# Optimization experiments

Hardware: AMD Instinct MI355X
Metric: run time of the kernel (lower is better)

Reference implementation:

```python
import jax, jax.numpy as jnp
import numpy as np

RADIUS = 0.2  # radius_cutoff
EPS_H = 1e-6
EPS_T = 1e-8
NUM_KNOTS = 16


def setup_inputs() -> dict:
    key = jax.random.key(0)
    ks = jax.random.split(key, 10)
    B, N, C = 2, 48 * 48, 16
    x = jax.random.normal(ks[0], (B, N, C), jnp.float32)
    phi_w1 = jax.random.normal(ks[1], (4, 32), jnp.float32) * 0.5
    phi_b1 = jax.random.normal(ks[2], (32,), jnp.float32) * 0.1
    phi_w2 = jax.random.normal(ks[3], (32, 1), jnp.float32) * 0.2
    phi_b2 = jax.random.normal(ks[4], (1,), jnp.float32) * 0.1
    h_w1 = jax.random.normal(ks[5], (2, 32), jnp.float32) * 0.5
    h_b1 = jax.random.normal(ks[6], (32,), jnp.float32) * 0.1
    h_w2 = jax.random.normal(ks[7], (32, 1), jnp.float32) * 0.2
    h_b2 = jax.random.normal(ks[8], (1,), jnp.float32) * 0.1
    S_m = jax.random.normal(ks[9], (NUM_KNOTS,), jnp.float32)
    return dict(x=x, phi_w1=phi_w1, phi_b1=phi_b1, phi_w2=phi_w2, phi_b2=phi_b2,
                h_w1=h_w1, h_b1=h_b1, h_w2=h_w2, h_b2=h_b2, S_m=S_m)


def _radial_spline(r, S_m):
    K = S_m.shape[0]
    knots = jnp.linspace(0.0, 1.0, K)
    r = jnp.clip(r, 0.0, 1.0)
    idx = jnp.clip(jnp.floor(r * (K - 1)).astype(jnp.int32), 0, K - 2)
    t_k = knots[idx]
    t_k1 = knots[idx + 1]
    wr = (r - t_k) / (t_k1 - t_k + EPS_T)
    return (1.0 - wr) * S_m[idx] + wr * S_m[idx + 1]


def reference(x, phi_w1, phi_b1, phi_w2, phi_b2, h_w1, h_b1, h_w2, h_b2, S_m):
    B, N, C = x.shape
    H = int(N ** 0.5)
    lin = jnp.linspace(0.0, 1.0, H)
    gx, gy = jnp.meshgrid(lin, lin, indexing='ij')
    coords = jnp.stack([gx, gy], axis=-1).reshape(N, 2)  # identical for every batch element

    # dense pairwise distances + radius mask  [N, N]
    diff = coords[:, None, :] - coords[None, :, :]
    dist = jnp.sqrt(jnp.sum(diff * diff, axis=-1))
    mask = (dist <= RADIUS).astype(x.dtype)

    # h_net: per-query bandwidth, Softplus(Linear(ReLU(Linear(coords))))  [N]
    h = jax.nn.softplus(jax.nn.relu(coords @ h_w1 + h_b1) @ h_w2 + h_b2)[:, 0]
    r_scaled = dist / (h[:, None] + EPS_H)
    psi = _radial_spline(r_scaled, S_m) * mask  # [N, N]

    # phi_net on all (x_i, y_j) coord pairs; original only fills masked entries,
    # elsewhere phi stays 0 -> dense eval then mask is the same math.  [N, N]
    xy = jnp.concatenate([jnp.broadcast_to(coords[:, None, :], (N, N, 2)),
                          jnp.broadcast_to(coords[None, :, :], (N, N, 2))], axis=-1)
    phi = (jax.nn.relu(xy @ phi_w1 + phi_b1) @ phi_w2 + phi_b2)[..., 0] * mask

    weights = phi * psi  # [N, N], same for every batch element
    norm = jnp.maximum(jnp.sum(mask, axis=-1, keepdims=True), 1.0)  # [N, 1]
    # sum_j weights[i,j] * x[b,j,c] / norm[i]  -- avoids materializing [B,N,N,C]
    out = jnp.einsum('ij,bjc->bic', weights, x) / norm[None, :, :]
    return out
```

## Files before the change

kernel.cpp:

```cpp
#include <hip/hip_runtime.h>
#include <cmath>

namespace {
constexpr int HG = 48;
constexpr int NP = HG * HG;
constexpr int CH = 16;
constexpr int WIN = 19;
constexpr int WIN2 = WIN * WIN;
constexpr float RADIUS = 0.2f;
constexpr float EPS_H = 1e-6f;
constexpr float EPS_T = 1e-8f;
constexpr int KNOTS = 16;
constexpr int PPB = 4;
constexpr int NCAND = 6;
}

__device__ __forceinline__ float lin48(int t) {
    return (t == HG - 1) ? 1.0f : (float)t * (1.0f / 47.0f);
}

__device__ __forceinline__ float softplus_f(float v) {
    return fmaxf(v, 0.0f) + log1pf(expf(-fabsf(v)));
}

__device__ __forceinline__ void wave_lds_fence() {
    __asm__ volatile("s_waitcnt lgkmcnt(0)" ::: "memory");
}

__global__ __launch_bounds__(256)
void si_blocks_kernel(const float* __restrict__ x,
                      const float* __restrict__ phi_w1,
                      const float* __restrict__ phi_b1,
                      const float* __restrict__ phi_w2,
                      const float* __restrict__ phi_b2,
                      const float* __restrict__ h_w1,
                      const float* __restrict__ h_b1,
                      const float* __restrict__ h_w2,
                      const float* __restrict__ h_b2,
                      const float* __restrict__ S_m,
                      float* __restrict__ out)
{
    const int tid  = threadIdx.x;
    const int lane = tid & 63;
    const int wv   = tid >> 6;
    const int i    = blockIdx.x * PPB + wv;
    const int ri   = i / HG;
    const int ci   = i - ri * HG;
    const float xi = lin48(ri);
    const float yi = lin48(ci);

    __shared__ float4 s_pq[PPB][32];
    __shared__ float  s_Sm[PPB][KNOTS];
    __shared__ float  s_w[PPB][WIN2];

    if (lane < 32) {
        const float pre = xi * phi_w1[lane] + yi * phi_w1[32 + lane] + phi_b1[lane];
        s_pq[wv][lane] = make_float4(pre, phi_w1[64 + lane], phi_w1[96 + lane],
                                     phi_w2[lane]);
    }
    if (lane < KNOTS) s_Sm[wv][lane] = S_m[lane];

    float hval;
    {
        const int k = lane & 31;
        float t = fmaxf(xi * h_w1[k] + yi * h_w1[32 + k] + h_b1[k], 0.0f) * h_w2[k];
        #pragma unroll
        for (int m = 1; m < 32; m <<= 1) t += __shfl_xor(t, m, 64);
        hval = softplus_f(t + h_b2[0]) + EPS_H;
    }
    const float b2    = phi_b2[0];
    const float rhinv = 1.0f / hval;

    wave_lds_fence();

    float xjv[NCAND], yjv[NCAND], pw[NCAND], accp[NCAND];
    float cnt = 0.0f;

    #pragma unroll
    for (int s = 0; s < NCAND; ++s) {
        const int t  = lane + 64 * s;
        const int tt = (t < WIN2) ? t : 0;
        const int a  = tt / WIN;
        const int bb = tt - a * WIN;
        const int rj = ri + a - 9;
        const int cj = ci + bb - 9;
        const bool valid = (t < WIN2) &&
                           ((unsigned)rj < (unsigned)HG) &&
                           ((unsigned)cj < (unsigned)HG);
        const int rjc = min(max(rj, 0), HG - 1);
        const int cjc = min(max(cj, 0), HG - 1);
        const float xx = lin48(rjc);
        const float yy = lin48(cjc);
        const float dx = xi - xx;
        const float dy = yi - yy;
        const float dist = sqrtf(dx * dx + dy * dy);
        const float m = (valid && dist <= RADIUS) ? 1.0f : 0.0f;
        cnt += m;

        float r = fminf(dist * rhinv, 1.0f);
        int idx = (int)(r * (float)(KNOTS - 1));
        idx = idx > (KNOTS - 2) ? (KNOTS - 2) : idx;
        const float tk  = (float)idx * (1.0f / (float)(KNOTS - 1));
        const float tk1 = (idx == KNOTS - 2) ? 1.0f
                        : (float)(idx + 1) * (1.0f / (float)(KNOTS - 1));
        const float wr  = (r - tk) / (tk1 - tk + EPS_T);
        const float psi = (1.0f - wr) * s_Sm[wv][idx] + wr * s_Sm[wv][idx + 1];

        pw[s]   = psi * m;
        xjv[s]  = xx;
        yjv[s]  = yy;
        accp[s] = b2;
    }

    #pragma unroll
    for (int m = 1; m < 64; m <<= 1) cnt += __shfl_xor(cnt, m, 64);
    const float rnorm = 1.0f / fmaxf(cnt, 1.0f);

    #pragma unroll
    for (int k = 0; k < 32; ++k) {
        const float4 q = s_pq[wv][k];
        #pragma unroll
        for (int s = 0; s < NCAND; ++s) {
            const float hk = fmaf(xjv[s], q.y, fmaf(yjv[s], q.z, q.x));
            accp[s] = fmaf(fmaxf(hk, 0.0f), q.w, accp[s]);
        }
    }

    #pragma unroll
    for (int s = 0; s < NCAND; ++s) {
        const int t = lane + 64 * s;
        if (t < WIN2) s_w[wv][t] = accp[s] * pw[s] * rnorm;
    }

    wave_lds_fence();

    const int rep = lane >> 3;
    const int pc  = lane & 7;
    const int b   = pc >> 2;
    const int c4  = pc & 3;
    const float* xb = x + b * NP * CH + c4 * 4;

    float4 acc = make_float4(0.0f, 0.0f, 0.0f, 0.0f);
    int t = rep, a = 0, bb = rep;
    #pragma unroll 8
    for (int n = 0; n < 46; ++n) {
        if (t < WIN2) {
            const int rj  = ri + a - 9;
            const int cj  = ci + bb - 9;
            const int rjc = min(max(rj, 0), HG - 1);
            const int cjc = min(max(cj, 0), HG - 1);
            const int j   = rjc * HG + cjc;
            const float wgt = s_w[wv][t];
            const float4 xv = *(const float4*)(xb + j * CH);
            acc.x = fmaf(wgt, xv.x, acc.x);
            acc.y = fmaf(wgt, xv.y, acc.y);
            acc.z = fmaf(wgt, xv.z, acc.z);
            acc.w = fmaf(wgt, xv.w, acc.w);
        }
        t += 8;
        bb += 8;
        const int ov = (bb >= WIN) ? 1 : 0;
        bb -= ov * WIN;
        a  += ov;
    }

    #pragma unroll
    for (int off = 8; off < 64; off <<= 1) {
        acc.x += __shfl_down(acc.x, off, 64);
        acc.y += __shfl_down(acc.y, off, 64);
        acc.z += __shfl_down(acc.z, off, 64);
        acc.w += __shfl_down(acc.w, off, 64);
    }

    if (rep == 0) {
        *(float4*)(out + (size_t)(b * NP + i) * CH + c4 * 4) = acc;
    }
}

extern "C" void kernel_launch(void* const* d_in, const int* in_sizes, int n_in,
                              void* d_out, int out_size, void* d_ws, size_t ws_size,
                              hipStream_t stream) {
    const float* x      = (const float*)d_in[0];
    const float* phi_w1 = (const float*)d_in[1];
    const float* phi_b1 = (const float*)d_in[2];
    const float* phi_w2 = (const float*)d_in[3];
    const float* phi_b2 = (const float*)d_in[4];
    const float* h_w1   = (const float*)d_in[5];
    const float* h_b1   = (const float*)d_in[6];
    const float* h_w2   = (const float*)d_in[7];
    const float* h_b2   = (const float*)d_in[8];
    const float* S_m    = (const float*)d_in[9];
    float* out          = (float*)d_out;

    si_blocks_kernel<<<dim3(NP / PPB), dim3(256), 0, stream>>>(
        x, phi_w1, phi_b1, phi_w2, phi_b2,
        h_w1, h_b1, h_w2, h_b2, S_m, out);
}
```

Before: 88.78 us.

## Use one 256-thread block per query point instead of one wave per point

Each block now handles a single query point, and its four waves share the 361-entry window. Weight computation is split across 256 threads (2 candidates each instead of 6), the neighbour count uses ballot/popcount, and the gather loop is split across waves with a cross-wave LDS reduction and a final normalise. The aim is to shorten the per-point critical path and launch 4x more blocks for parallelism. In exchange it adds block-wide barriers and recomputes the h_net and shared setup four times as often.

```diff
diff --git a/kernel.cpp b/kernel.cpp
--- a/kernel.cpp
+++ b/kernel.cpp
@@ -11,8 +11,6 @@
 constexpr float EPS_H = 1e-6f;
 constexpr float EPS_T = 1e-8f;
 constexpr int KNOTS = 16;
-constexpr int PPB = 4;
-constexpr int NCAND = 6;
 }
 
 __device__ __forceinline__ float lin48(int t) {
@@ -21,10 +19,6 @@
 
 __device__ __forceinline__ float softplus_f(float v) {
     return fmaxf(v, 0.0f) + log1pf(expf(-fabsf(v)));
-}
-
-__device__ __forceinline__ void wave_lds_fence() {
-    __asm__ volatile("s_waitcnt lgkmcnt(0)" ::: "memory");
 }
 
 __global__ __launch_bounds__(256)
@@ -43,22 +37,24 @@
     const int tid  = threadIdx.x;
     const int lane = tid & 63;
     const int wv   = tid >> 6;
-    const int i    = blockIdx.x * PPB + wv;
+    const int i    = blockIdx.x;
     const int ri   = i / HG;
     const int ci   = i - ri * HG;
     const float xi = lin48(ri);
     const float yi = lin48(ci);
 
-    __shared__ float4 s_pq[PPB][32];
-    __shared__ float  s_Sm[PPB][KNOTS];
-    __shared__ float  s_w[PPB][WIN2];
+    __shared__ float4 s_pq[32];
+    __shared__ float  s_Sm[KNOTS];
+    __shared__ float  s_w[WIN2];
+    __shared__ float4 s_part[4][8];
+    __shared__ float  s_cnt[4];
 
-    if (lane < 32) {
-        const float pre = xi * phi_w1[lane] + yi * phi_w1[32 + lane] + phi_b1[lane];
-        s_pq[wv][lane] = make_float4(pre, phi_w1[64 + lane], phi_w1[96 + lane],
-                                     phi_w2[lane]);
+    if (tid < 32) {
+        const float pre = xi * phi_w1[tid] + yi * phi_w1[32 + tid] + phi_b1[tid];
+        s_pq[tid] = make_float4(pre, phi_w1[64 + tid], phi_w1[96 + tid], phi_w2[tid]);
+    } else if (tid < 32 + KNOTS) {
+        s_Sm[tid - 32] = S_m[tid - 32];
     }
-    if (lane < KNOTS) s_Sm[wv][lane] = S_m[lane];
 
     float hval;
     {
@@ -68,25 +64,23 @@
         for (int m = 1; m < 32; m <<= 1) t += __shfl_xor(t, m, 64);
         hval = softplus_f(t + h_b2[0]) + EPS_H;
     }
+    const float rhinv = 1.0f / hval;
     const float b2    = phi_b2[0];
-    const float rhinv = 1.0f / hval;
 
-    wave_lds_fence();
+    __syncthreads();
 
-    float xjv[NCAND], yjv[NCAND], pw[NCAND], accp[NCAND];
     float cnt = 0.0f;
-
     #pragma unroll
-    for (int s = 0; s < NCAND; ++s) {
-        const int t  = lane + 64 * s;
-        const int tt = (t < WIN2) ? t : 0;
+    for (int s = 0; s < 2; ++s) {
+        const int t  = tid + 256 * s;
+        const bool in = (t < WIN2);
+        const int tt = in ? t : 0;
         const int a  = tt / WIN;
         const int bb = tt - a * WIN;
         const int rj = ri + a - 9;
         const int cj = ci + bb - 9;
-        const bool valid = (t < WIN2) &&
-                           ((unsigned)rj < (unsigned)HG) &&
-                           ((unsigned)cj < (unsigned)HG);
+        const bool valid = in && ((unsigned)rj < (unsigned)HG) &&
+                                 ((unsigned)cj < (unsigned)HG);
         const int rjc = min(max(rj, 0), HG - 1);
         const int cjc = min(max(cj, 0), HG - 1);
         const float xx = lin48(rjc);
@@ -94,8 +88,10 @@
         const float dx = xi - xx;
         const float dy = yi - yy;
         const float dist = sqrtf(dx * dx + dy * dy);
-        const float m = (valid && dist <= RADIUS) ? 1.0f : 0.0f;
-        cnt += m;
+        const bool hit = valid && (dist <= RADIUS);
+
+        const unsigned long long bal = __ballot(hit);
+        cnt = fmaf(1.0f, (float)__popcll(bal), cnt);
 
         float r = fminf(dist * rhinv, 1.0f);
         int idx = (int)(r * (float)(KNOTS - 1));
@@ -104,64 +100,51 @@
         const float tk1 = (idx == KNOTS - 2) ? 1.0f
                         : (float)(idx + 1) * (1.0f / (float)(KNOTS - 1));
         const float wr  = (r - tk) / (tk1 - tk + EPS_T);
-        const float psi = (1.0f - wr) * s_Sm[wv][idx] + wr * s_Sm[wv][idx + 1];
+        const float psi = (1.0f - wr) * s_Sm[idx] + wr * s_Sm[idx + 1];
 
-        pw[s]   = psi * m;
-        xjv[s]  = xx;
-        yjv[s]  = yy;
-        accp[s] = b2;
+        float p0 = b2, p1 = 0.0f;
+        #pragma unroll
+        for (int k = 0; k < 32; k += 2) {
+            const float4 q0 = s_pq[k];
+            const float4 q1 = s_pq[k + 1];
+            const float h0 = fmaf(xx, q0.y, fmaf(yy, q0.z, q0.x));
+            const float h1 = fmaf(xx, q1.y, fmaf(yy, q1.z, q1.x));
+            p0 = fmaf(fmaxf(h0, 0.0f), q0.w, p0);
+            p1 = fmaf(fmaxf(h1, 0.0f), q1.w, p1);
+        }
+        if (in) s_w[t] = hit ? (p0 + p1) * psi : 0.0f;
     }
+    if (lane == 0) s_cnt[wv] = cnt;
 
-    #pragma unroll
-    for (int m = 1; m < 64; m <<= 1) cnt += __shfl_xor(cnt, m, 64);
-    const float rnorm = 1.0f / fmaxf(cnt, 1.0f);
+    __syncthreads();
 
-    #pragma unroll
-    for (int k = 0; k < 32; ++k) {
-        const float4 q = s_pq[wv][k];
-        #pragma unroll
-        for (int s = 0; s < NCAND; ++s) {
-            const float hk = fmaf(xjv[s], q.y, fmaf(yjv[s], q.z, q.x));
-            accp[s] = fmaf(fmaxf(hk, 0.0f), q.w, accp[s]);
-        }
-    }
-
-    #pragma unroll
-    for (int s = 0; s < NCAND; ++s) {
-        const int t = lane + 64 * s;
-        if (t < WIN2) s_w[wv][t] = accp[s] * pw[s] * rnorm;
-    }
-
-    wave_lds_fence();
-
-    const int rep = lane >> 3;
-    const int pc  = lane & 7;
-    const int b   = pc >> 2;
-    const int c4  = pc & 3;
+    const int rep   = lane >> 3;
+    const int rep32 = wv * 8 + rep;
+    const int pc    = lane & 7;
+    const int b     = pc >> 2;
+    const int c4    = pc & 3;
     const float* xb = x + b * NP * CH + c4 * 4;
 
     float4 acc = make_float4(0.0f, 0.0f, 0.0f, 0.0f);
-    int t = rep, a = 0, bb = rep;
-    #pragma unroll 8
-    for (int n = 0; n < 46; ++n) {
+    int t  = rep32;
+    int a  = (rep32 >= WIN) ? 1 : 0;
+    int bb = rep32 - a * WIN;
+    #pragma unroll
+    for (int n = 0; n < 12; ++n) {
         if (t < WIN2) {
-            const int rj  = ri + a - 9;
-            const int cj  = ci + bb - 9;
-            const int rjc = min(max(rj, 0), HG - 1);
-            const int cjc = min(max(cj, 0), HG - 1);
+            const int rjc = min(max(ri + a - 9, 0), HG - 1);
+            const int cjc = min(max(ci + bb - 9, 0), HG - 1);
             const int j   = rjc * HG + cjc;
-            const float wgt = s_w[wv][t];
+            const float wgt = s_w[t];
             const float4 xv = *(const float4*)(xb + j * CH);
             acc.x = fmaf(wgt, xv.x, acc.x);
             acc.y = fmaf(wgt, xv.y, acc.y);
             acc.z = fmaf(wgt, xv.z, acc.z);
             acc.w = fmaf(wgt, xv.w, acc.w);
         }
-        t += 8;
-        bb += 8;
-        const int ov = (bb >= WIN) ? 1 : 0;
-        bb -= ov * WIN;
-        a  += ov;
+        t += 32;
+        bb += 13; a += 1;
+        if (bb >= WIN) { bb -= WIN; a += 1; }
     }
 
     #pragma unroll
@@ -171,9 +154,25 @@
         acc.z += __shfl_down(acc.z, off, 64);
         acc.w += __shfl_down(acc.w, off, 64);
     }
+    if (rep == 0) s_part[wv][pc] = acc;
 
-    if (rep == 0) {
-        *(float4*)(out + (size_t)(b * NP + i) * CH + c4 * 4) = acc;
+    __syncthreads();
+
+    if (tid < 8) {
+        const float4 a0 = s_part[0][tid];
+        const float4 a1 = s_part[1][tid];
+        const float4 a2 = s_part[2][tid];
+        const float4 a3 = s_part[3][tid];
+        const float ctot = s_cnt[0] + s_cnt[1] + s_cnt[2] + s_cnt[3];
+        const float rnorm = 1.0f / fmaxf(ctot, 1.0f);
+        float4 r;
+        r.x = (a0.x + a1.x + a2.x + a3.x) * rnorm;
+        r.y = (a0.y + a1.y + a2.y + a3.y) * rnorm;
+        r.z = (a0.z + a1.z + a2.z + a3.z) * rnorm;
+        r.w = (a0.w + a1.w + a2.w + a3.w) * rnorm;
+        const int bo = tid >> 2;
+        const int co = tid & 3;
+        *(float4*)(out + (size_t)(bo * NP + i) * CH + co * 4) = r;
     }
 }
 
@@ -192,7 +191,7 @@
     const float* S_m    = (const float*)d_in[9];
     float* out          = (float*)d_out;
 
-    si_blocks_kernel<<<dim3(NP / PPB), dim3(256), 0, stream>>>(
+    si_blocks_kernel<<<dim3(NP), dim3(256), 0, stream>>>(
         x, phi_w1, phi_b1, phi_w2, phi_b2,
         h_w1, h_b1, h_w2, h_b2, S_m, out);
 }
```

After: 83.67 us. -5.8%, faster.
